# Kernel tuning notes

Hardware: AMD Instinct MI355X
Metric: run time of the kernel (lower is better)

The kernel has to match this reference:

```python
import jax, jax.numpy as jnp
import numpy as np

B, L, DIN = 2048, 70, 15
HID, NF, K = 16, 4, 40          # hidden_units//2, n_features, kernel_size
C = DIN + 1 + NF                # 20 signature input channels (original + time + conv features)
Z0 = 64
SIG_CH = C + C * C + C ** 3     # 8420, depth-3 signature channels


def setup_inputs() -> dict:
    key = jax.random.key(0)
    ks = jax.random.split(key, 8)
    return {
        "observed_data": jax.random.normal(ks[0], (B, L, DIN), jnp.float32),
        "observed_tp": jnp.linspace(0.0, 1.0, L, dtype=jnp.float32),
        "conv1_w": jax.random.normal(ks[1], (HID, DIN, K), jnp.float32) / np.float32(np.sqrt(DIN * K)),
        "conv1_b": jnp.zeros((HID,), jnp.float32),
        "conv2_w": jax.random.normal(ks[2], (HID, HID), jnp.float32) / np.float32(np.sqrt(HID)),
        "conv2_b": jnp.zeros((HID,), jnp.float32),
        "conv3_w": jax.random.normal(ks[3], (NF, HID), jnp.float32) / np.float32(np.sqrt(HID)),
        "conv3_b": jnp.zeros((NF,), jnp.float32),
        "w_out": jax.random.normal(ks[4], (2 * Z0, SIG_CH), jnp.float32) * np.float32(np.sqrt(2.0 / (SIG_CH + 2 * Z0))),
        "b_out": jnp.zeros((2 * Z0,), jnp.float32),
    }


def _augment(x, w1, b1, w2, b2, w3, b3):
    # x: (B, L, DIN).  signatory.Augment: conv(K) -> relu -> conv1x1 -> relu -> conv1x1,
    # then concat [truncated original, time channel, conv features] along channels.
    xc = jnp.transpose(x, (0, 2, 1))                                   # (B, DIN, L)
    h = jax.lax.conv_general_dilated(xc, w1, (1,), 'VALID')            # (B, HID, Lp)
    h = h + b1[None, :, None]
    h = jnp.einsum('oc,bcl->bol', w2, jax.nn.relu(h)) + b2[None, :, None]
    h = jnp.einsum('oc,bcl->bol', w3, jax.nn.relu(h)) + b3[None, :, None]
    conv_out = jnp.transpose(h, (0, 2, 1))                             # (B, Lp, NF)
    Lp = conv_out.shape[1]
    orig = x[:, K - 1:, :]                                             # (B, Lp, DIN)
    t = jnp.linspace(0.0, 1.0, Lp, dtype=x.dtype)
    time = jnp.broadcast_to(t[None, :, None], (x.shape[0], Lp, 1))
    return jnp.concatenate([orig, time, conv_out], axis=2)             # (B, Lp, C)


def _signature_depth3(path):
    # Truncated (depth 3) path signature with basepoint=True, via Chen's identity:
    # S <- S \otimes exp(dx) over increments, zero basepoint prepended.
    incs = jnp.diff(path, axis=1, prepend=jnp.zeros_like(path[:, :1]))  # (B, Lp, C)
    incs = jnp.transpose(incs, (1, 0, 2))                               # (Lp, B, C)
    Bn, Cn = path.shape[0], path.shape[2]
    s1 = jnp.zeros((Bn, Cn), path.dtype)
    s2 = jnp.zeros((Bn, Cn, Cn), path.dtype)
    s3 = jnp.zeros((Bn, Cn, Cn, Cn), path.dtype)

    def step(carry, d):
        s1, s2, s3 = carry
        e2 = 0.5 * d[:, :, None] * d[:, None, :]                        # d\otimes d / 2
        e3 = (e2[:, :, :, None] * d[:, None, None, :]) / 3.0            # d^{\otimes 3} / 6
        n3 = (s3
              + s2[:, :, :, None] * d[:, None, None, :]
              + s1[:, :, None, None] * e2[:, None, :, :]
              + e3)
        n2 = s2 + s1[:, :, None] * d[:, None, :] + e2
        n1 = s1 + d
        return (n1, n2, n3), None

    (s1, s2, s3), _ = jax.lax.scan(step, (s1, s2, s3), incs)
    return jnp.concatenate([s1, s2.reshape(Bn, -1), s3.reshape(Bn, -1)], axis=1)


def reference(observed_data, observed_tp, conv1_w, conv1_b, conv2_w, conv2_b,
              conv3_w, conv3_b, w_out, b_out):
    # encode_obs_time=False -> observed_tp unused
    path = _augment(observed_data, conv1_w, conv1_b, conv2_w, conv2_b, conv3_w, conv3_b)
    sig = _signature_depth3(path)                                       # (B, SIG_CH)
    z = sig @ w_out.T + b_out                                           # (B, 2*Z0)
    mean_z0 = z[:, :Z0][None]                                           # (1, B, Z0)
    std_z0 = jax.nn.softplus(z[:, Z0:][None])                           # (1, B, Z0)
    return mean_z0, std_z0
```

## Files before the change

### kernel.cpp

```cpp
#include <hip/hip_runtime.h>
#include <math.h>

#define B_TOT 2048
#define D_INC 15
#define KW    40
#define CCH   20
#define LP    31
#define SIGCH 8420
#define SIGP  8448
#define NOUT  128
#define KSPLIT 11
#define KLEN  768

typedef _Float16 f16;
typedef _Float16 f16x8 __attribute__((ext_vector_type(8)));
typedef _Float16 f16x4 __attribute__((ext_vector_type(4)));
typedef float    f32x4 __attribute__((ext_vector_type(4)));

__global__ __launch_bounds__(256) void k_augsig(
    const float* __restrict__ x,  const float* __restrict__ w1, const float* __restrict__ b1,
    const float* __restrict__ w2, const float* __restrict__ b2,
    const float* __restrict__ w3, const float* __restrict__ b3,
    const float* __restrict__ w_out, f16* __restrict__ wh, f16* __restrict__ sig)
{
    if (blockIdx.x >= 512) {
        int t0 = (blockIdx.x - 512) * 256 + threadIdx.x;
        for (int chunk = t0; chunk < 128 * 1056; chunk += 8192) {
            int o  = chunk / 1056;
            int cw = chunk - o * 1056;
            int c0 = cw * 8;
            f16x8 v;
            if (c0 + 8 <= SIGCH) {
                const float* src = w_out + (size_t)o * SIGCH + c0;
                float4 a = *(const float4*)src;
                float4 b = *(const float4*)(src + 4);
                v = (f16x8){(f16)a.x,(f16)a.y,(f16)a.z,(f16)a.w,
                            (f16)b.x,(f16)b.y,(f16)b.z,(f16)b.w};
            } else {
#pragma unroll
                for (int e = 0; e < 8; ++e) {
                    int c = c0 + e;
                    v[e] = (c < SIGCH) ? (f16)w_out[(size_t)o * SIGCH + c] : (f16)0.f;
                }
            }
            *(f16x8*)(wh + (size_t)o * SIGP + c0) = v;
        }
        return;
    }

    __shared__ float xs[4 * 1068];
    __shared__ float w1s[9600];
    __shared__ float wsmall[356];
    float* w2s = wsmall;        float* b2s = wsmall + 256;
    float* w3s = wsmall + 272;  float* b3s = wsmall + 336;
    float* b1s = wsmall + 340;
    float* h1s   = w1s;
    float* pprev = w1s + 2624;
    float* incs  = w1s + 5248;

    const int tid = threadIdx.x;
    const int b0  = blockIdx.x * 4;

    for (int i = tid; i < 4 * 1050; i += 256) {
        int bl = i / 1050; int t = i - bl * 1050;
        xs[bl * 1068 + t] = x[(size_t)b0 * 1050 + i];
    }
    for (int i = tid; i < 9600; i += 256) {
        int h = i / 600; int m = i - h * 600;
        w1s[m * 16 + h] = w1[i];
    }
    if (tid < 256) w2s[tid] = w2[tid];
    if (tid < 16)  b2s[tid] = b2[tid];
    if (tid < 64)  w3s[tid] = w3[tid];
    if (tid < 4)   b3s[tid] = b3[tid];
    if (tid < 16)  b1s[tid] = b1[tid];
    __syncthreads();

    {
        const int h     = tid & 15;
        const int qr    = (tid >> 4) & 3;
        const int bl    = tid >> 6;
        const int pbase = qr * 8;
        float acc[8];
#pragma unroll
        for (int p = 0; p < 8; ++p) acc[p] = 0.f;
        for (int c = 0; c < D_INC; ++c) {
            float xcol[47];
            const int base = bl * 1068 + pbase * 15 + c;
#pragma unroll
            for (int i = 0; i < 47; ++i) xcol[i] = xs[base + i * 15];
#pragma unroll
            for (int k = 0; k < KW; ++k) {
                const float wv = w1s[(c * 40 + k) * 16 + h];
#pragma unroll
                for (int p = 0; p < 8; ++p) acc[p] += xcol[p + k] * wv;
            }
        }
        __syncthreads();
        const float bb1 = b1s[h];
#pragma unroll
        for (int p = 0; p < 8; ++p) {
            int pos = pbase + p;
            if (pos < LP) h1s[(bl * 31 + pos) * 17 + h] = fmaxf(acc[p] + bb1, 0.f);
        }
        __syncthreads();
    }

    if (tid < 124) {
        const int bl2 = tid / 31;
        const int pos = tid - bl2 * 31;
        float hr[16];
#pragma unroll
        for (int c2 = 0; c2 < 16; ++c2) hr[c2] = h1s[tid * 17 + c2];
        float h2[16];
#pragma unroll
        for (int o = 0; o < 16; ++o) {
            float s = b2s[o];
#pragma unroll
            for (int c2 = 0; c2 < 16; ++c2) s += w2s[o * 16 + c2] * hr[c2];
            h2[o] = fmaxf(s, 0.f);
        }
        float h3[4];
#pragma unroll
        for (int f = 0; f < 4; ++f) {
            float s = b3s[f];
#pragma unroll
            for (int c2 = 0; c2 < 16; ++c2) s += w3s[f * 16 + c2] * h2[c2];
            h3[f] = s;
        }
        float* pr = pprev + bl2 * 656 + 20 + pos * 20;
#pragma unroll
        for (int d = 0; d < D_INC; ++d) pr[d] = xs[bl2 * 1068 + (pos + 39) * 15 + d];
        pr[15] = (float)pos * (1.0f / 30.0f);
#pragma unroll
        for (int f = 0; f < 4; ++f) pr[16 + f] = h3[f];
    } else {
        int z = tid - 124;
        if (z < 80) pprev[(z / 20) * 656 + (z % 20)] = 0.f;
    }
    __syncthreads();

    const int lane = tid & 63;
    const int w    = tid >> 6;
    const int b    = b0 + w;
    float* pp = pprev + w * 656;
    float* ic = incs  + w * 624;

    for (int i = lane; i < 620; i += 64) ic[i] = pp[20 + i] - pp[i];
    __syncthreads();

    int iv[7], jv[7];
#pragma unroll
    for (int q = 0; q < 7; ++q) {
        int p = lane + 64 * q;
        iv[q] = p / 20; jv[q] = p - iv[q] * 20;
    }
    float s2r[7];
    float s3r[7][20];
#pragma unroll
    for (int q = 0; q < 7; ++q) {
        s2r[q] = 0.f;
#pragma unroll
        for (int k = 0; k < 20; ++k) s3r[q][k] = 0.f;
    }

    for (int t = 0; t < LP; ++t) {
        const float* ip = &ic[t * 20];
        const float* sp = &pp[t * 20];
        float dreg[20];
        const float4* dp = (const float4*)ip;
#pragma unroll
        for (int r = 0; r < 5; ++r) {
            float4 v = dp[r];
            dreg[4*r] = v.x; dreg[4*r+1] = v.y; dreg[4*r+2] = v.z; dreg[4*r+3] = v.w;
        }
#pragma unroll
        for (int q = 0; q < 7; ++q) {
            if (lane + 64 * q < 400) {
                const float di  = ip[iv[q]];
                const float dj  = ip[jv[q]];
                const float s1i = sp[iv[q]];
                const float t2  = s2r[q] + (0.5f * s1i + (1.0f / 6.0f) * di) * dj;
#pragma unroll
                for (int k = 0; k < 20; ++k) s3r[q][k] += t2 * dreg[k];
                s2r[q] += (s1i + 0.5f * di) * dj;
            }
        }
    }

    f16* sg = sig + (size_t)b * SIGP;
    if (lane < 20) sg[lane] = (f16)pp[620 + lane];
#pragma unroll
    for (int q = 0; q < 6; ++q) sg[20 + q * 64 + lane] = (f16)s2r[q];
    if (lane < 16) sg[404 + lane] = (f16)s2r[6];
#pragma unroll
    for (int q = 0; q < 7; ++q) {
        int p = lane + 64 * q;
        if (p < 400) {
            f16* base = sg + 420 + p * 20;
#pragma unroll
            for (int g = 0; g < 5; ++g) {
                f16x4 v = { (f16)s3r[q][4*g],   (f16)s3r[q][4*g+1],
                            (f16)s3r[q][4*g+2], (f16)s3r[q][4*g+3] };
                *(f16x4*)(base + 4 * g) = v;
            }
        }
    }
    if (lane < 28) sg[SIGCH + lane] = (f16)0.f;
}

__global__ __launch_bounds__(256) void k_gemm(const f16* __restrict__ sigh,
                                              const f16* __restrict__ wh,
                                              float* __restrict__ z_part)
{
    __shared__ f16 As[2048];
    __shared__ f16 Bs[8192];
    const int tid = threadIdx.x;
    const int l   = tid & 63;
    const int wv  = tid >> 6;
    const int mt  = blockIdx.x / KSPLIT;
    const int s   = blockIdx.x - mt * KSPLIT;
    const int m0  = mt * 32;
    const int kb  = s * KLEN;

    const f32x4 z4 = {0.f, 0.f, 0.f, 0.f};
    f32x4 acc[2][2];
    acc[0][0] = z4; acc[0][1] = z4; acc[1][0] = z4; acc[1][1] = z4;

    const size_t gA = (size_t)(m0 + (tid & 31)) * SIGP + kb + (tid >> 5) * 8;
    size_t gB[4];
#pragma unroll
    for (int r = 0; r < 4; ++r) {
        int slot = r * 256 + tid;
        gB[r] = (size_t)(slot & 127) * SIGP + kb + (slot >> 7) * 8;
    }

    f16x8 aR = *(const f16x8*)(sigh + gA);
    f16x8 bR[4];
#pragma unroll
    for (int r = 0; r < 4; ++r) bR[r] = *(const f16x8*)(wh + gB[r]);

    const int kg   = l >> 4;
    const int mrow = l & 15;

    for (int ch = 0; ch < 12; ++ch) {
        *(f16x8*)&As[tid * 8] = aR;
#pragma unroll
        for (int r = 0; r < 4; ++r) *(f16x8*)&Bs[(r * 256 + tid) * 8] = bR[r];
        __syncthreads();

        if (ch < 11) {
            int koff = (ch + 1) * 64;
            aR = *(const f16x8*)(sigh + gA + koff);
#pragma unroll
            for (int r = 0; r < 4; ++r) bR[r] = *(const f16x8*)(wh + gB[r] + koff);
        }

#pragma unroll
        for (int kc = 0; kc < 2; ++kc) {
            f16x8 aF[2], bF[2];
#pragma unroll
            for (int m2 = 0; m2 < 2; ++m2)
                aF[m2] = *(const f16x8*)&As[((kc * 4 + kg) * 32 + m2 * 16 + mrow) * 8];
#pragma unroll
            for (int n2 = 0; n2 < 2; ++n2)
                bF[n2] = *(const f16x8*)&Bs[((kc * 4 + kg) * 128 + wv * 32 + n2 * 16 + mrow) * 8];
#pragma unroll
            for (int m2 = 0; m2 < 2; ++m2)
#pragma unroll
                for (int n2 = 0; n2 < 2; ++n2)
                    acc[m2][n2] = __builtin_amdgcn_mfma_f32_16x16x32_f16(aF[m2], bF[n2], acc[m2][n2], 0, 0, 0);
        }
        __syncthreads();
    }

#pragma unroll
    for (int m2 = 0; m2 < 2; ++m2) {
#pragma unroll
        for (int n2 = 0; n2 < 2; ++n2) {
            int n = wv * 32 + n2 * 16 + (l & 15);
#pragma unroll
            for (int r = 0; r < 4; ++r) {
                int m = m0 + m2 * 16 + (l >> 4) * 4 + r;
                z_part[((size_t)s * B_TOT + m) * NOUT + n] = acc[m2][n2][r];
            }
        }
    }
}

__global__ __launch_bounds__(256) void k_final(const float* __restrict__ z_part,
                                               const float* __restrict__ b_out,
                                               float* __restrict__ out)
{
    int idx = blockIdx.x * 256 + threadIdx.x;
    int b = idx >> 7;
    int o = idx & 127;
    float z = b_out[o];
#pragma unroll
    for (int s = 0; s < KSPLIT; ++s) z += z_part[((size_t)s * B_TOT + b) * NOUT + o];
    if (o < 64) {
        out[(size_t)b * 64 + o] = z;
    } else {
        float sp = fmaxf(z, 0.f) + log1pf(expf(-fabsf(z)));
        out[131072 + (size_t)b * 64 + (o - 64)] = sp;
    }
}

extern "C" void kernel_launch(void* const* d_in, const int* in_sizes, int n_in,
                              void* d_out, int out_size, void* d_ws, size_t ws_size,
                              hipStream_t stream)
{
    const float* x     = (const float*)d_in[0];
    const float* w1    = (const float*)d_in[2];
    const float* b1    = (const float*)d_in[3];
    const float* w2    = (const float*)d_in[4];
    const float* b2    = (const float*)d_in[5];
    const float* w3    = (const float*)d_in[6];
    const float* b3    = (const float*)d_in[7];
    const float* w_out = (const float*)d_in[8];
    const float* b_out = (const float*)d_in[9];
    float* out = (float*)d_out;

    float* ws    = (float*)d_ws;
    f16*   sigh  = (f16*)ws;
    f16*   wh    = (f16*)(ws + 8650752);
    float* zpart = ws + 9191424;

    hipLaunchKernelGGL(k_augsig, dim3(544),  dim3(256), 0, stream,
                       x, w1, b1, w2, b2, w3, b3, w_out, wh, sigh);
    hipLaunchKernelGGL(k_gemm,   dim3(704),  dim3(256), 0, stream, sigh, wh, zpart);
    hipLaunchKernelGGL(k_final,  dim3(1024), dim3(256), 0, stream, zpart, b_out, out);
}
```

Baseline: 158.6 us.

## Compute conv1 with f16 MFMA and pack signature accumulation as float2

The 40-tap conv1 used to be a scalar FP32 loop over shared-memory weights. It now runs as f16 MFMA 16x16x32 tiles. A new single-block prep kernel repacks w1 into an f16 fragment layout, and x is converted to padded f16 rows in shared memory. The large w1 staging buffer goes away, which cuts shared memory so the kernel can declare two blocks per CU. The depth-3 accumulation is rewritten with float2 vectors so the compiler can emit packed FMA. Costs are f16 precision in the conv, one extra kernel launch, and more register pressure from holding 20 weight fragments.

After: 154.0 us. -2.9%, faster.

```diff
diff --git a/kernel.cpp b/kernel.cpp
--- a/kernel.cpp
+++ b/kernel.cpp
@@ -16,9 +16,31 @@
 typedef _Float16 f16x8 __attribute__((ext_vector_type(8)));
 typedef _Float16 f16x4 __attribute__((ext_vector_type(4)));
 typedef float    f32x4 __attribute__((ext_vector_type(4)));
-
-__global__ __launch_bounds__(256) void k_augsig(
-    const float* __restrict__ x,  const float* __restrict__ w1, const float* __restrict__ b1,
+typedef float    f32x2 __attribute__((ext_vector_type(2)));
+
+__global__ __launch_bounds__(256) void k_prep(const float* __restrict__ w1,
+                                              f16* __restrict__ wA)
+{
+    const int ln = threadIdx.x & 63;
+    const int wv = threadIdx.x >> 6;
+    const int h  = ln & 15;
+    const int q4 = ln >> 4;
+    for (int gi = 0; gi < 5; ++gi) {
+        int g = wv * 5 + gi;
+        f16x8 v;
+#pragma unroll
+        for (int j = 0; j < 8; ++j) {
+            int kq = q4 * 8 + j;
+            int kk = 2 * g + (kq >> 4);
+            int c  = kq & 15;
+            v[j] = (c < D_INC) ? (f16)w1[h * 600 + c * 40 + kk] : (f16)0.f;
+        }
+        *(f16x8*)(wA + g * 512 + ln * 8) = v;
+    }
+}
+
+__global__ __launch_bounds__(256, 2) void k_augsig(
+    const float* __restrict__ x,  const f16* __restrict__ wA, const float* __restrict__ b1,
     const float* __restrict__ w2, const float* __restrict__ b2,
     const float* __restrict__ w3, const float* __restrict__ b3,
     const float* __restrict__ w_out, f16* __restrict__ wh, f16* __restrict__ sig)
@@ -49,14 +71,14 @@
     }
 
     __shared__ float xs[4 * 1068];
-    __shared__ float w1s[9600];
+    __shared__ f16   xp16[4 * 1152];
+    __shared__ float pprev[4 * 656];
     __shared__ float wsmall[356];
     float* w2s = wsmall;        float* b2s = wsmall + 256;
     float* w3s = wsmall + 272;  float* b3s = wsmall + 336;
     float* b1s = wsmall + 340;
-    float* h1s   = w1s;
-    float* pprev = w1s + 2624;
-    float* incs  = w1s + 5248;
+    float* h1s  = (float*)xp16;
+    float* incs = xs;
 
     const int tid = threadIdx.x;
     const int b0  = blockIdx.x * 4;
@@ -64,10 +86,6 @@
     for (int i = tid; i < 4 * 1050; i += 256) {
         int bl = i / 1050; int t = i - bl * 1050;
         xs[bl * 1068 + t] = x[(size_t)b0 * 1050 + i];
-    }
-    for (int i = tid; i < 9600; i += 256) {
-        int h = i / 600; int m = i - h * 600;
-        w1s[m * 16 + h] = w1[i];
     }
     if (tid < 256) w2s[tid] = w2[tid];
     if (tid < 16)  b2s[tid] = b2[tid];
@@ -76,35 +94,50 @@
     if (tid < 16)  b1s[tid] = b1[tid];
     __syncthreads();
 
-    {
-        const int h     = tid & 15;
-        const int qr    = (tid >> 4) & 3;
-        const int bl    = tid >> 6;
-        const int pbase = qr * 8;
-        float acc[8];
-#pragma unroll
-        for (int p = 0; p < 8; ++p) acc[p] = 0.f;
-        for (int c = 0; c < D_INC; ++c) {
-            float xcol[47];
-            const int base = bl * 1068 + pbase * 15 + c;
-#pragma unroll
-            for (int i = 0; i < 47; ++i) xcol[i] = xs[base + i * 15];
-#pragma unroll
-            for (int k = 0; k < KW; ++k) {
-                const float wv = w1s[(c * 40 + k) * 16 + h];
-#pragma unroll
-                for (int p = 0; p < 8; ++p) acc[p] += xcol[p + k] * wv;
-            }
-        }
-        __syncthreads();
-        const float bb1 = b1s[h];
-#pragma unroll
-        for (int p = 0; p < 8; ++p) {
-            int pos = pbase + p;
-            if (pos < LP) h1s[(bl * 31 + pos) * 17 + h] = fmaxf(acc[p] + bb1, 0.f);
-        }
-        __syncthreads();
-    }
+    for (int r = tid; r < 280; r += 256) {
+        int bl = r / 70; int pos = r - bl * 70;
+        const float* src = xs + bl * 1068 + pos * 15;
+        f16* dst = xp16 + bl * 1152 + pos * 16;
+#pragma unroll
+        for (int c = 0; c < 15; ++c) dst[c] = (f16)src[c];
+        dst[15] = (f16)0.f;
+    }
+    __syncthreads();
+
+    const int lane = tid & 63;
+    const int w    = tid >> 6;
+    const int n16  = lane & 15;
+    const int q4   = lane >> 4;
+
+    f16x8 wa[20];
+#pragma unroll
+    for (int g = 0; g < 20; ++g) wa[g] = *(const f16x8*)(wA + g * 512 + lane * 8);
+
+    f32x4 cacc[2];
+#pragma unroll
+    for (int tile = 0; tile < 2; ++tile) {
+        const int pos0 = tile * 15;
+        f32x4 acc = {0.f, 0.f, 0.f, 0.f};
+#pragma unroll
+        for (int g = 0; g < 20; ++g) {
+            const f16x8 bf = *(const f16x8*)&xp16[w * 1152 +
+                (pos0 + n16 + 2 * g + (q4 >> 1)) * 16 + (q4 & 1) * 8];
+            acc = __builtin_amdgcn_mfma_f32_16x16x32_f16(wa[g], bf, acc, 0, 0, 0);
+        }
+        cacc[tile] = acc;
+    }
+    __syncthreads();
+
+#pragma unroll
+    for (int tile = 0; tile < 2; ++tile) {
+        int pos = tile * 15 + n16;
+#pragma unroll
+        for (int r = 0; r < 4; ++r) {
+            int h = q4 * 4 + r;
+            h1s[(w * 31 + pos) * 17 + h] = fmaxf(cacc[tile][r] + b1s[h], 0.f);
+        }
+    }
+    __syncthreads();
 
     if (tid < 124) {
         const int bl2 = tid / 31;
@@ -140,12 +173,8 @@
     }
     __syncthreads();
 
-    const int lane = tid & 63;
-    const int w    = tid >> 6;
-    const int b    = b0 + w;
     float* pp = pprev + w * 656;
     float* ic = incs  + w * 624;
-
     for (int i = lane; i < 620; i += 64) ic[i] = pp[20 + i] - pp[i];
     __syncthreads();
 
@@ -156,23 +185,24 @@
         iv[q] = p / 20; jv[q] = p - iv[q] * 20;
     }
     float s2r[7];
-    float s3r[7][20];
+    f32x2 s3v[7][10];
 #pragma unroll
     for (int q = 0; q < 7; ++q) {
         s2r[q] = 0.f;
 #pragma unroll
-        for (int k = 0; k < 20; ++k) s3r[q][k] = 0.f;
+        for (int k = 0; k < 10; ++k) s3v[q][k] = (f32x2){0.f, 0.f};
     }
 
     for (int t = 0; t < LP; ++t) {
         const float* ip = &ic[t * 20];
         const float* sp = &pp[t * 20];
-        float dreg[20];
+        f32x2 dv[10];
         const float4* dp = (const float4*)ip;
 #pragma unroll
         for (int r = 0; r < 5; ++r) {
             float4 v = dp[r];
-            dreg[4*r] = v.x; dreg[4*r+1] = v.y; dreg[4*r+2] = v.z; dreg[4*r+3] = v.w;
+            dv[2*r]   = (f32x2){v.x, v.y};
+            dv[2*r+1] = (f32x2){v.z, v.w};
         }
 #pragma unroll
         for (int q = 0; q < 7; ++q) {
@@ -181,13 +211,15 @@
                 const float dj  = ip[jv[q]];
                 const float s1i = sp[iv[q]];
                 const float t2  = s2r[q] + (0.5f * s1i + (1.0f / 6.0f) * di) * dj;
-#pragma unroll
-                for (int k = 0; k < 20; ++k) s3r[q][k] += t2 * dreg[k];
+                const f32x2 t2v = {t2, t2};
+#pragma unroll
+                for (int k = 0; k < 10; ++k) s3v[q][k] += t2v * dv[k];
                 s2r[q] += (s1i + 0.5f * di) * dj;
             }
         }
     }
 
+    const int b = b0 + w;
     f16* sg = sig + (size_t)b * SIGP;
     if (lane < 20) sg[lane] = (f16)pp[620 + lane];
 #pragma unroll
@@ -200,8 +232,8 @@
             f16* base = sg + 420 + p * 20;
 #pragma unroll
             for (int g = 0; g < 5; ++g) {
-                f16x4 v = { (f16)s3r[q][4*g],   (f16)s3r[q][4*g+1],
-                            (f16)s3r[q][4*g+2], (f16)s3r[q][4*g+3] };
+                f16x4 v = { (f16)s3v[q][2*g][0],   (f16)s3v[q][2*g][1],
+                            (f16)s3v[q][2*g+1][0], (f16)s3v[q][2*g+1][1] };
                 *(f16x4*)(base + 4 * g) = v;
             }
         }
@@ -324,10 +356,12 @@
     float* ws    = (float*)d_ws;
     f16*   sigh  = (f16*)ws;
     f16*   wh    = (f16*)(ws + 8650752);
-    float* zpart = ws + 9191424;
-
+    f16*   wA    = (f16*)(ws + 9191424);
+    float* zpart = ws + 9196544;
+
+    hipLaunchKernelGGL(k_prep,   dim3(1),    dim3(256), 0, stream, w1, wA);
     hipLaunchKernelGGL(k_augsig, dim3(544),  dim3(256), 0, stream,
-                       x, w1, b1, w2, b2, w3, b3, w_out, wh, sigh);
+                       x, wA, b1, w2, b2, w3, b3, w_out, wh, sigh);
     hipLaunchKernelGGL(k_gemm,   dim3(704),  dim3(256), 0, stream, sigh, wh, zpart);
     hipLaunchKernelGGL(k_final,  dim3(1024), dim3(256), 0, stream, zpart, b_out, out);
 }
```
